# Kernel tuning notes

Hardware: AMD Instinct MI355X
Metric: run time of the kernel (lower is better)

Reference implementation:

```python
import jax, jax.numpy as jnp
import numpy as np

B, T, N_IN, N = 64, 512, 256, 512

def setup_inputs() -> dict:
    key = jax.random.key(0)
    k1, k2, k3 = jax.random.split(key, 3)
    x = jax.random.normal(k1, (B, T, N_IN), dtype=jnp.float32)
    # match nn.Linear default init scale roughly (uniform +-1/sqrt(fan_in))
    W_ih = jax.random.uniform(k2, (N, N_IN), dtype=jnp.float32, minval=-1.0, maxval=1.0) / np.sqrt(N_IN)
    W_hh = jax.random.uniform(k3, (N, N), dtype=jnp.float32, minval=-1.0, maxval=1.0) / np.sqrt(N)
    return {"x": x, "W_ih": W_ih, "W_hh": W_hh}

def reference(x, W_ih, W_hh):
    # h_t = W_hh @ tanh(h_{t-1}) + W_ih @ x_t, h_0 = 0 (pre-activation hidden stored)
    # x: [B, T, n_in] (batch_first). Precompute input projections for all steps.
    xp = jnp.einsum('btc,nc->tbn', x, W_ih)  # [T, B, N]

    def step(h, xp_t):
        h_new = jnp.tanh(h) @ W_hh.T + xp_t  # [B, N]
        return h_new, h_new

    h0 = jnp.zeros((x.shape[0], W_hh.shape[0]), dtype=x.dtype)
    _, hs = jax.lax.scan(step, h0, xp)  # hs: [T, B, N]
    return jnp.swapaxes(hs, 0, 1)  # [B, T, N], batch_first output
```

## Files before the change

kernel.cpp:

```cpp
#include <hip/hip_runtime.h>
#include <hip/hip_bf16.h>
#include <stdint.h>

#define B_   64
#define T_   512
#define NIN_ 256
#define N_   512

typedef _Float16 half2_t __attribute__((ext_vector_type(2)));

#if defined(__has_builtin)
#if __has_builtin(__builtin_amdgcn_fdot2)
#define HAVE_FDOT2 1
#endif
#endif

__device__ __forceinline__ float dot2acc(unsigned int a, unsigned int b, float c) {
#ifdef HAVE_FDOT2
  return __builtin_amdgcn_fdot2(__builtin_bit_cast(half2_t, a),
                                __builtin_bit_cast(half2_t, b), c, false);
#else
  half2_t ha = __builtin_bit_cast(half2_t, a), hb = __builtin_bit_cast(half2_t, b);
  c += (float)ha[0] * (float)hb[0];
  c += (float)ha[1] * (float)hb[1];
  return c;
#endif
}

__device__ __forceinline__ float fast_tanh(float x) {
  float e = __expf(2.0f * x);
  return 1.0f - 2.0f / (e + 1.0f);
}

__device__ __forceinline__ unsigned int packh2(float a, float b) {
  half2_t h;
  h[0] = (_Float16)a;
  h[1] = (_Float16)b;
  return __builtin_bit_cast(unsigned int, h);
}

__device__ __forceinline__ int thp_idx(int p) {
  return (((p >> 2) & 15) << 4) + ((p >> 6) << 2) + (p & 3);
}

__global__ __launch_bounds__(256) void xproj(const float* __restrict__ x,
                                             const float* __restrict__ Wih,
                                             float* __restrict__ out) {
  const int tid = threadIdx.x;
  const int bm = blockIdx.x;
  const int bn = blockIdx.y;
  const int tm = tid & 15;
  const int tn = tid >> 4;
  const int m0 = bm << 7;
  const int n0 = bn << 7;

  __shared__ float xt[32][132];
  __shared__ float wt[32][132];

  float acc[8][8];
#pragma unroll
  for (int i = 0; i < 8; ++i)
#pragma unroll
    for (int j = 0; j < 8; ++j) acc[i][j] = 0.f;

  for (int ko = 0; ko < NIN_; ko += 32) {
#pragma unroll
    for (int it = 0; it < 4; ++it) {
      const int fidx = it * 256 + tid;
      const int mm = fidx >> 3;
      const int k4 = (fidx & 7) << 2;
      const float4 vx = *(const float4*)(x + (size_t)(m0 + mm) * NIN_ + ko + k4);
      xt[k4 + 0][mm] = vx.x; xt[k4 + 1][mm] = vx.y;
      xt[k4 + 2][mm] = vx.z; xt[k4 + 3][mm] = vx.w;
      const float4 vw = *(const float4*)(Wih + (size_t)(n0 + mm) * NIN_ + ko + k4);
      wt[k4 + 0][mm] = vw.x; wt[k4 + 1][mm] = vw.y;
      wt[k4 + 2][mm] = vw.z; wt[k4 + 3][mm] = vw.w;
    }
    __syncthreads();
#pragma unroll 4
    for (int kk = 0; kk < 32; ++kk) {
      float a[8], b[8];
      *(float4*)&a[0] = *(const float4*)&xt[kk][8 * tm];
      *(float4*)&a[4] = *(const float4*)&xt[kk][8 * tm + 4];
      *(float4*)&b[0] = *(const float4*)&wt[kk][8 * tn];
      *(float4*)&b[4] = *(const float4*)&wt[kk][8 * tn + 4];
#pragma unroll
      for (int i = 0; i < 8; ++i)
#pragma unroll
        for (int j = 0; j < 8; ++j) acc[i][j] = fmaf(a[i], b[j], acc[i][j]);
    }
    __syncthreads();
  }

#pragma unroll
  for (int i = 0; i < 8; ++i) {
    float4 v0 = make_float4(acc[i][0], acc[i][1], acc[i][2], acc[i][3]);
    float4 v1 = make_float4(acc[i][4], acc[i][5], acc[i][6], acc[i][7]);
    float* p = out + (size_t)(m0 + 8 * tm + i) * N_ + n0 + 8 * tn;
    *(float4*)p = v0;
    *((float4*)p + 1) = v1;
  }
}

__global__ __launch_bounds__(512) void rnn_scan(const float* __restrict__ Whh,
                                                float* __restrict__ out,
                                                unsigned long long* __restrict__ ex) {
  const int blk = blockIdx.x;
  const int xcd = blk & 7;
  const int rest = blk >> 3;
  const int m = rest & 3;
  const int b = xcd + ((rest >> 2) << 3);
  const int tid = threadIdx.x;
  const int wv = tid >> 6;
  const int lane = tid & 63;
  const int q = lane & 3;
  const int nn = wv * 16 + (lane >> 2);
  const int gn = m * 128 + nn;

  __shared__ __align__(16) unsigned int thp[2][256];

  float* outb = out + (size_t)b * T_ * N_;
  unsigned long long* exb = ex + (size_t)b * 1024;

  unsigned int w[64];
  {
    const float* wr = Whh + (size_t)gn * N_ + q * 128;
#pragma unroll
    for (int j = 0; j < 64; ++j) {
      float2 v = *(const float2*)(wr + 2 * j);
      w[j] = packh2(v.x, v.y);
    }
  }

  if (tid < 256) {
    float2 h0 = *(const float2*)(outb + 2 * tid);
    thp[0][thp_idx(tid)] = packh2(fast_tanh(h0.x), fast_tanh(h0.y));
  }

  const int pv = tid & 127;
  const int sr = tid >> 7;
  const int sm = sr + (sr >= m ? 1 : 0);
  const int prn = sm * 128 + pv;

  __syncthreads();

  for (int t = 1; t < T_; ++t) {
    float xp = 0.f;
    if (q == 0) xp = outb[(size_t)t * N_ + gn];

    if (t >= 2 && tid < 384) {
      unsigned long long v;
      do {
        v = __hip_atomic_load(&exb[((t - 1) & 1) * 512 + prn],
                              __ATOMIC_RELAXED, __HIP_MEMORY_SCOPE_AGENT);
      } while ((unsigned int)(v >> 32) != (unsigned int)(t - 1));
      const float th = fast_tanh(__uint_as_float((unsigned int)v));
      const float thn = __shfl_xor(th, 1);
      if ((tid & 1) == 0) thp[(t - 1) & 1][thp_idx(prn >> 1)] = packh2(th, thn);
    }
    __syncthreads();

    const uint4* tq = (const uint4*)&thp[(t - 1) & 1][0];
    float acc = 0.f;
#pragma unroll
    for (int j4 = 0; j4 < 16; ++j4) {
      const uint4 tv = tq[j4 * 4 + q];
      acc = dot2acc(w[4 * j4 + 0], tv.x, acc);
      acc = dot2acc(w[4 * j4 + 1], tv.y, acc);
      acc = dot2acc(w[4 * j4 + 2], tv.z, acc);
      acc = dot2acc(w[4 * j4 + 3], tv.w, acc);
    }
    acc += __shfl_xor(acc, 1);
    acc += __shfl_xor(acc, 2);

    float th_own = 0.f;
    if (q == 0) {
      const float y = acc + xp;
      __hip_atomic_store(&exb[(t & 1) * 512 + gn],
                         ((unsigned long long)(unsigned int)t << 32) |
                             (unsigned long long)__float_as_uint(y),
                         __ATOMIC_RELAXED, __HIP_MEMORY_SCOPE_AGENT);
      __builtin_nontemporal_store(y, &outb[(size_t)t * N_ + gn]);
      th_own = fast_tanh(y);
    }
    const float th_nb = __shfl_xor(th_own, 4);
    if ((lane & 7) == 0)
      thp[t & 1][thp_idx(gn >> 1)] = packh2(th_own, th_nb);
  }
}

extern "C" void kernel_launch(void* const* d_in, const int* in_sizes, int n_in,
                              void* d_out, int out_size, void* d_ws, size_t ws_size,
                              hipStream_t stream) {
  const float* x   = (const float*)d_in[0];
  const float* Wih = (const float*)d_in[1];
  const float* Whh = (const float*)d_in[2];
  float* out = (float*)d_out;
  unsigned long long* ex = (unsigned long long*)d_ws;

  hipMemsetAsync(d_ws, 0, (size_t)B_ * 2 * 512 * 8, stream);

  dim3 g1(256, 4);
  xproj<<<g1, 256, 0, stream>>>(x, Wih, out);
  rnn_scan<<<256, 512, 0, stream>>>(Whh, out, ex);
}
```

Before: 760.2 us.

## Fuse input projection into scan kernel with chunked producer-consumer overlap

Merges the input-projection GEMM and the recurrent scan into one persistent launch. 192 extra blocks compute projection tiles in time-chunk order and signal per-chunk counters, and the 256 scan blocks wait on each 128-step chunk before using it. The goal is to hide the projection GEMM and one launch behind the serial recurrence. In exchange it relies on all 448 blocks being co-resident, adds spin-waits, and the GEMM tile shrinks to 8x4 per thread.

Measured after the change: 1.153 ms. 1.52x slower.

```diff
diff --git a/kernel.cpp b/kernel.cpp
--- a/kernel.cpp
+++ b/kernel.cpp
@@ -1,5 +1,4 @@
 #include <hip/hip_runtime.h>
-#include <hip/hip_bf16.h>
 #include <stdint.h>
 
 #define B_   64
@@ -31,11 +30,8 @@
   float e = __expf(2.0f * x);
   return 1.0f - 2.0f / (e + 1.0f);
 }
-
 __device__ __forceinline__ unsigned int packh2(float a, float b) {
-  half2_t h;
-  h[0] = (_Float16)a;
-  h[1] = (_Float16)b;
+  half2_t h; h[0] = (_Float16)a; h[1] = (_Float16)b;
   return __builtin_bit_cast(unsigned int, h);
 }
 
@@ -43,74 +39,78 @@
   return (((p >> 2) & 15) << 4) + ((p >> 6) << 2) + (p & 3);
 }
 
-__global__ __launch_bounds__(256) void xproj(const float* __restrict__ x,
-                                             const float* __restrict__ Wih,
-                                             float* __restrict__ out) {
+__global__ __launch_bounds__(512, 4) void rnn_fused(
+    const float* __restrict__ x, const float* __restrict__ Wih,
+    const float* __restrict__ Whh, float* __restrict__ out,
+    unsigned long long* __restrict__ ex, int* __restrict__ ctrl) {
+  const int blk = blockIdx.x;
   const int tid = threadIdx.x;
-  const int bm = blockIdx.x;
-  const int bn = blockIdx.y;
-  const int tm = tid & 15;
-  const int tn = tid >> 4;
-  const int m0 = bm << 7;
-  const int n0 = bn << 7;
-
-  __shared__ float xt[32][132];
-  __shared__ float wt[32][132];
-
-  float acc[8][8];
-#pragma unroll
-  for (int i = 0; i < 8; ++i)
-#pragma unroll
-    for (int j = 0; j < 8; ++j) acc[i][j] = 0.f;
-
-  for (int ko = 0; ko < NIN_; ko += 32) {
-#pragma unroll
-    for (int it = 0; it < 4; ++it) {
-      const int fidx = it * 256 + tid;
-      const int mm = fidx >> 3;
-      const int k4 = (fidx & 7) << 2;
-      const float4 vx = *(const float4*)(x + (size_t)(m0 + mm) * NIN_ + ko + k4);
-      xt[k4 + 0][mm] = vx.x; xt[k4 + 1][mm] = vx.y;
-      xt[k4 + 2][mm] = vx.z; xt[k4 + 3][mm] = vx.w;
-      const float4 vw = *(const float4*)(Wih + (size_t)(n0 + mm) * NIN_ + ko + k4);
-      wt[k4 + 0][mm] = vw.x; wt[k4 + 1][mm] = vw.y;
-      wt[k4 + 2][mm] = vw.z; wt[k4 + 3][mm] = vw.w;
-    }
-    __syncthreads();
+
+  if (blk >= 256) {
+    __shared__ float xt[32][132];
+    __shared__ float wt[32][132];
+    const int tm2 = tid >> 5;
+    const int tn2 = tid & 31;
+    for (int tau = blk - 256; tau < 1024; tau += 192) {
+      const int tc = tau >> 8;
+      const int j  = tau & 255;
+      const int bb = j >> 2;
+      const int bn = j & 3;
+      const int bm = bb * 4 + tc;
+      const int m0 = bm << 7;
+      const int nn0 = bn << 7;
+
+      float acc[8][4];
+#pragma unroll
+      for (int i = 0; i < 8; ++i)
+#pragma unroll
+        for (int jj = 0; jj < 4; ++jj) acc[i][jj] = 0.f;
+
+      for (int ko2 = 0; ko2 < NIN_; ko2 += 32) {
+#pragma unroll
+        for (int it = 0; it < 2; ++it) {
+          const int fidx = it * 512 + tid;
+          const int mm = fidx >> 3;
+          const int k4 = (fidx & 7) << 2;
+          const float4 vx = *(const float4*)(x + (size_t)(m0 + mm) * NIN_ + ko2 + k4);
+          xt[k4 + 0][mm] = vx.x; xt[k4 + 1][mm] = vx.y;
+          xt[k4 + 2][mm] = vx.z; xt[k4 + 3][mm] = vx.w;
+          const float4 vw = *(const float4*)(Wih + (size_t)(nn0 + mm) * NIN_ + ko2 + k4);
+          wt[k4 + 0][mm] = vw.x; wt[k4 + 1][mm] = vw.y;
+          wt[k4 + 2][mm] = vw.z; wt[k4 + 3][mm] = vw.w;
+        }
+        __syncthreads();
 #pragma unroll 4
-    for (int kk = 0; kk < 32; ++kk) {
-      float a[8], b[8];
-      *(float4*)&a[0] = *(const float4*)&xt[kk][8 * tm];
-      *(float4*)&a[4] = *(const float4*)&xt[kk][8 * tm + 4];
-      *(float4*)&b[0] = *(const float4*)&wt[kk][8 * tn];
-      *(float4*)&b[4] = *(const float4*)&wt[kk][8 * tn + 4];
+        for (int kk = 0; kk < 32; ++kk) {
+          float a[8], bb2[4];
+          *(float4*)&a[0] = *(const float4*)&xt[kk][8 * tm2];
+          *(float4*)&a[4] = *(const float4*)&xt[kk][8 * tm2 + 4];
+          *(float4*)&bb2[0] = *(const float4*)&wt[kk][4 * tn2];
+#pragma unroll
+          for (int i = 0; i < 8; ++i)
+#pragma unroll
+            for (int jj = 0; jj < 4; ++jj)
+              acc[i][jj] = fmaf(a[i], bb2[jj], acc[i][jj]);
+        }
+        __syncthreads();
+      }
 #pragma unroll
       for (int i = 0; i < 8; ++i)
-#pragma unroll
-        for (int j = 0; j < 8; ++j) acc[i][j] = fmaf(a[i], b[j], acc[i][j]);
-    }
-    __syncthreads();
-  }
-
-#pragma unroll
-  for (int i = 0; i < 8; ++i) {
-    float4 v0 = make_float4(acc[i][0], acc[i][1], acc[i][2], acc[i][3]);
-    float4 v1 = make_float4(acc[i][4], acc[i][5], acc[i][6], acc[i][7]);
-    float* p = out + (size_t)(m0 + 8 * tm + i) * N_ + n0 + 8 * tn;
-    *(float4*)p = v0;
-    *((float4*)p + 1) = v1;
-  }
-}
-
-__global__ __launch_bounds__(512) void rnn_scan(const float* __restrict__ Whh,
-                                                float* __restrict__ out,
-                                                unsigned long long* __restrict__ ex) {
-  const int blk = blockIdx.x;
+        *(float4*)(out + (size_t)(m0 + 8 * tm2 + i) * N_ + nn0 + 4 * tn2) =
+            make_float4(acc[i][0], acc[i][1], acc[i][2], acc[i][3]);
+      __threadfence();
+      __syncthreads();
+      if (tid == 0)
+        __hip_atomic_fetch_add(&ctrl[tc], 1, __ATOMIC_RELEASE,
+                               __HIP_MEMORY_SCOPE_AGENT);
+    }
+    return;
+  }
+
   const int xcd = blk & 7;
   const int rest = blk >> 3;
   const int m = rest & 3;
   const int b = xcd + ((rest >> 2) << 3);
-  const int tid = threadIdx.x;
   const int wv = tid >> 6;
   const int lane = tid & 63;
   const int q = lane & 3;
@@ -132,6 +132,13 @@
     }
   }
 
+  if (tid == 0) {
+    while (__hip_atomic_load(&ctrl[0], __ATOMIC_ACQUIRE,
+                             __HIP_MEMORY_SCOPE_AGENT) < 256)
+      __builtin_amdgcn_s_sleep(1);
+  }
+  __syncthreads();
+
   if (tid < 256) {
     float2 h0 = *(const float2*)(outb + 2 * tid);
     thp[0][thp_idx(tid)] = packh2(fast_tanh(h0.x), fast_tanh(h0.y));
@@ -145,6 +152,15 @@
   __syncthreads();
 
   for (int t = 1; t < T_; ++t) {
+    if ((t & 127) == 0) {
+      if (tid == 0) {
+        while (__hip_atomic_load(&ctrl[t >> 7], __ATOMIC_ACQUIRE,
+                                 __HIP_MEMORY_SCOPE_AGENT) < 256)
+          __builtin_amdgcn_s_sleep(1);
+      }
+      __syncthreads();
+    }
+
     float xp = 0.f;
     if (q == 0) xp = outb[(size_t)t * N_ + gn];
 
@@ -197,10 +213,8 @@
   const float* Whh = (const float*)d_in[2];
   float* out = (float*)d_out;
   unsigned long long* ex = (unsigned long long*)d_ws;
-
-  hipMemsetAsync(d_ws, 0, (size_t)B_ * 2 * 512 * 8, stream);
-
-  dim3 g1(256, 4);
-  xproj<<<g1, 256, 0, stream>>>(x, Wih, out);
-  rnn_scan<<<256, 512, 0, stream>>>(Whh, out, ex);
-}
+  int* ctrl = (int*)((char*)d_ws + 524288);
+
+  hipMemsetAsync(d_ws, 0, 524288 + 64, stream);
+  rnn_fused<<<448, 512, 0, stream>>>(x, Wih, Whh, out, ex, ctrl);
+}
```
